# Performance work log

Measured on AMD Instinct MI355X. Metric: run time of the kernel, lower is better.

## Reference

```python
import jax, jax.numpy as jnp
import numpy as np

B = 4096      # Monte-Carlo trajectories (batch)
H = 100       # hidden_size = in_size - 1; also noise_size
T = 100       # num_timesteps
WIDTH = 256   # MLP width


def setup_inputs() -> dict:
    key = jax.random.key(0)
    ks = jax.random.split(key, 8)

    def lin(k, out_d, in_d):
        # eqx.nn.Linear default init: U(-1/sqrt(in), 1/sqrt(in)) for W and b
        lim = 1.0 / np.sqrt(in_d)
        kw, kb = jax.random.split(k)
        W = jax.random.uniform(kw, (out_d, in_d), minval=-lim, maxval=lim, dtype=jnp.float32)
        b = jax.random.uniform(kb, (out_d,), minval=-lim, maxval=lim, dtype=jnp.float32)
        return W, b

    W0, b0 = lin(ks[0], WIDTH, H + 1)
    W1, b1 = lin(ks[1], WIDTH, WIDTH)
    W2, b2 = lin(ks[2], WIDTH, WIDTH)
    W3, b3 = lin(ks[3], WIDTH, WIDTH)
    W4, b4 = lin(ks[4], 1, WIDTH)

    x0 = 1.0 + 0.1 * jax.random.normal(ks[5], (B, H), dtype=jnp.float32)
    t0 = jnp.zeros((1,), jnp.float32)
    dt = jnp.full((1,), 0.01, jnp.float32)
    return dict(x0=x0, t0=t0, dt=dt, num_timesteps=T,
                W0=W0, b0=b0, W1=W1, b1=b1, W2=W2, b2=b2, W3=W3, b3=b3, W4=W4, b4=b4)


def _mlp(params, t, x):
    # t: (1,) scalar time broadcast to batch; x: (B, H) -> (B, 1)
    W0, b0, W1, b1, W2, b2, W3, b3, W4, b4 = params
    inp = jnp.concatenate([jnp.broadcast_to(t, (x.shape[0], 1)), x], axis=-1)  # (B, H+1)
    h = jax.nn.relu(inp @ W0.T + b0)
    h = jax.nn.relu(h @ W1.T + b1)
    h = jax.nn.relu(h @ W2.T + b2)
    h = jax.nn.relu(h @ W3.T + b3)
    return h @ W4.T + b4  # (B, 1)


def _u_and_dudx(params, t, x):
    # y = u(t, x), z = du/dx via VJP with cotangent = ones (out_size == 1)
    y, vjp_fn = jax.vjp(lambda x_: _mlp(params, t, x_), x)
    (dudx,) = vjp_fn(jnp.ones_like(y))
    return y, dudx  # (B,1), (B,H)


def reference(x0, t0, dt, num_timesteps, W0, b0, W1, b1, W2, b2, W3, b3, W4, b4):
    params = (W0, b0, W1, b1, W2, b2, W3, b3, W4, b4)
    key = jax.random.key(42)
    sqdt = jnp.sqrt(dt)  # (1,)

    # initial y0, z0 evaluated at t = 0 (as in the original __call__)
    y0, z0 = _u_and_dudx(params, jnp.zeros((1,), x0.dtype), x0)

    def step(carry, _):
        i, x, y, z, k = carry
        k, k2 = jax.random.split(k)
        next_t = t0 + (i + 1.0) * dt                       # (1,)
        dW = jax.random.normal(k, x.shape, x.dtype) * sqdt  # noise_size == H
        sig = 0.4 * x                                       # sigma_fn
        x1 = x + sig * dW                                   # mu_fn == 0
        phi = 0.05 * (y - jnp.sum(x * z, axis=-1, keepdims=True))
        y1_tilde = y + phi * dt + jnp.sum(z * sig * dW, axis=-1, keepdims=True)
        y1, z1 = _u_and_dudx(params, next_t, x1)
        return (i + 1.0, x1, y1, z1, k2), (x1, y1_tilde, y1)

    carry0 = (jnp.zeros((), x0.dtype), x0, y0, z0, key)
    carry, outputs = jax.lax.scan(step, carry0, None, length=num_timesteps)
    # outputs = (xs (T,B,H), y_tildes (T,B,1), ys (T,B,1))
    return carry[1:4] + outputs  # drop step counter / key from returned carry
```

## Files before the change

kernel.cpp:

```cpp
#include <hip/hip_runtime.h>
#include <stdint.h>

#define B_TRAJ  4096
#define H_DIM   100
#define T_STEPS 100
#define ROWS    16
#define NBLK    256
#define THREADS 1024

typedef float    f32x4  __attribute__((ext_vector_type(4)));
typedef __bf16   bf16x8 __attribute__((ext_vector_type(8)));
typedef uint16_t u16x8  __attribute__((ext_vector_type(8)));
typedef uint8_t  u8x8   __attribute__((ext_vector_type(8)));

#define OB_P0F   0
#define OB_P1F   65536
#define OB_P2F   131072
#define OB_P3F   196608
#define OB_P1B   262144
#define OB_P2B   327680
#define OB_P3B   393216
#define OB_P0B   458752
#define OB_W4F8  491520
#define OB_KEYS  491776
#define PACK_TOTAL 459008
#define PACK_GRID ((PACK_TOTAL + 255) / 256)

#define WSCALE   32.0f
#define INV_WS   0.03125f
#define INV_ZS   2.44140625e-4f

__device__ __forceinline__ uint16_t f2bf(float f) {
  uint32_t u = __float_as_uint(f);
  uint32_t r = u + 0x7FFFu + ((u >> 16) & 1u);
  return (uint16_t)(r >> 16);
}
__device__ __forceinline__ float bf2f(uint16_t u) {
  return __uint_as_float(((uint32_t)u) << 16);
}
__device__ __forceinline__ uint8_t f2e4m3(float v) {
  int pk = __builtin_amdgcn_cvt_pk_fp8_f32(v, 0.0f, 0, false);
  return (uint8_t)(pk & 0xFF);
}
__device__ __forceinline__ uint32_t rotl32(uint32_t v, int d) {
  return (v << d) | (v >> (32 - d));
}

__device__ __forceinline__ void threefry2x32(uint32_t k0, uint32_t k1,
                                             uint32_t x0, uint32_t x1,
                                             uint32_t& o0, uint32_t& o1) {
  const uint32_t k2 = k0 ^ k1 ^ 0x1BD11BDAu;
  x0 += k0; x1 += k1;
  x0 += x1; x1 = rotl32(x1, 13); x1 ^= x0;
  x0 += x1; x1 = rotl32(x1, 15); x1 ^= x0;
  x0 += x1; x1 = rotl32(x1, 26); x1 ^= x0;
  x0 += x1; x1 = rotl32(x1,  6); x1 ^= x0;
  x0 += k1; x1 += k2 + 1u;
  x0 += x1; x1 = rotl32(x1, 17); x1 ^= x0;
  x0 += x1; x1 = rotl32(x1, 29); x1 ^= x0;
  x0 += x1; x1 = rotl32(x1, 16); x1 ^= x0;
  x0 += x1; x1 = rotl32(x1, 24); x1 ^= x0;
  x0 += k2; x1 += k0 + 2u;
  x0 += x1; x1 = rotl32(x1, 13); x1 ^= x0;
  x0 += x1; x1 = rotl32(x1, 15); x1 ^= x0;
  x0 += x1; x1 = rotl32(x1, 26); x1 ^= x0;
  x0 += x1; x1 = rotl32(x1,  6); x1 ^= x0;
  x0 += k0; x1 += k1 + 3u;
  x0 += x1; x1 = rotl32(x1, 17); x1 ^= x0;
  x0 += x1; x1 = rotl32(x1, 29); x1 ^= x0;
  x0 += x1; x1 = rotl32(x1, 16); x1 ^= x0;
  x0 += x1; x1 = rotl32(x1, 24); x1 ^= x0;
  x0 += k1; x1 += k2 + 4u;
  x0 += x1; x1 = rotl32(x1, 13); x1 ^= x0;
  x0 += x1; x1 = rotl32(x1, 15); x1 ^= x0;
  x0 += x1; x1 = rotl32(x1, 26); x1 ^= x0;
  x0 += x1; x1 = rotl32(x1,  6); x1 ^= x0;
  x0 += k2; x1 += k0 + 5u;
  o0 = x0; o1 = x1;
}

__device__ __forceinline__ float erfinv_f32(float x) {
  float w = -__logf(fmaf(-x, x, 1.0f));
  float p;
  if (w < 5.0f) {
    w = w - 2.5f;
    p = 2.81022636e-08f;
    p = fmaf(p, w, 3.43273939e-07f);
    p = fmaf(p, w, -3.5233877e-06f);
    p = fmaf(p, w, -4.39150654e-06f);
    p = fmaf(p, w, 0.00021858087f);
    p = fmaf(p, w, -0.00125372503f);
    p = fmaf(p, w, -0.00417768164f);
    p = fmaf(p, w, 0.246640727f);
    p = fmaf(p, w, 1.50140941f);
  } else {
    w = sqrtf(w) - 3.0f;
    p = -0.000200214257f;
    p = fmaf(p, w, 0.000100950558f);
    p = fmaf(p, w, 0.00134934322f);
    p = fmaf(p, w, -0.00367342844f);
    p = fmaf(p, w, 0.00573950773f);
    p = fmaf(p, w, -0.0076224613f);
    p = fmaf(p, w, 0.00943887047f);
    p = fmaf(p, w, 1.00167406f);
    p = fmaf(p, w, 2.83297682f);
  }
  return p * x;
}

__global__ __launch_bounds__(256) void pack_kernel(
    const float* __restrict__ W0, const float* __restrict__ W1,
    const float* __restrict__ W2, const float* __restrict__ W3,
    const float* __restrict__ W4, uint8_t* __restrict__ P) {
  const int i = blockIdx.x * 256 + threadIdx.x;
  if (i == 0) {
    uint32_t* K = (uint32_t*)(P + OB_KEYS);
    uint32_t c0 = 0u, c1 = 42u;
    for (int s = 0; s < T_STEPS; ++s) {
      uint32_t a0_, a1_, n0, n1;
      threefry2x32(c0, c1, 0u, 0u, a0_, a1_);
      threefry2x32(c0, c1, 0u, 1u, n0, n1);
      K[2 * s] = a0_; K[2 * s + 1] = a1_;
      c0 = n0; c1 = n1;
    }
  }
  if (i >= PACK_TOTAL) return;

  if (i < 32768) {
    const int e = i;
    const int kk = e & 31, n = (e >> 5) & 255, kt = e >> 13;
    const int k = kt * 32 + kk;
    const float v = (k < 101) ? W0[n * 101 + k] : 0.0f;
    ((uint16_t*)(P + OB_P0F))[e] = f2bf(v);
    return;
  }
  int j = i - 32768;
  if (j < 393216) {
    const int pk = j >> 16;
    const int e = j & 65535;
    const int kk = e & 31, n = (e >> 5) & 255, kt = e >> 13;
    const int k = kt * 32 + kk;
    float v;
    switch (pk) {
      case 0: v = W1[n * 256 + k]; break;
      case 1: v = W2[n * 256 + k]; break;
      case 2: v = W3[n * 256 + k]; break;
      case 3: v = W1[k * 256 + n]; break;
      case 4: v = W2[k * 256 + n]; break;
      default: v = W3[k * 256 + n]; break;
    }
    P[OB_P1F + j] = f2e4m3(v * WSCALE);
    return;
  }
  j -= 393216;
  if (j < 32768) {
    const int kk = j & 31, n = (j >> 5) & 127, kt = j >> 12;
    const int k = kt * 32 + kk;
    const float v = (n < 100) ? W0[k * 101 + 1 + n] : 0.0f;
    P[OB_P0B + j] = f2e4m3(v * WSCALE);
    return;
  }
  j -= 32768;
  P[OB_W4F8 + j] = f2e4m3(W4[j] * 128.0f);
}

struct SmemT {
  uint16_t actI[ROWS][136];
  uint8_t  act1[ROWS][264];
  uint8_t  act2[ROWS][264];
  uint8_t  act3[ROWS][264];
  uint8_t  act4[ROWS][264];
  uint8_t  dp4[ROWS][264];
  uint8_t  dpA[ROWS][264];
  uint8_t  dpB[ROWS][264];
  float x_s[ROWS * H_DIM];
  float z_s[ROWS * H_DIM];
  float dw_s[ROWS * H_DIM];
  float y_s[ROWS];
  uint32_t keyA[T_STEPS], keyB[T_STEPS];
};


__device__ __forceinline__ void gemm_fwd_f8(const uint8_t (*in)[264],
                                            const uint8_t* __restrict__ Pm,
                                            const float* __restrict__ bias,
                                            uint8_t (*outb)[264],
                                            int wave, int lane) {
  const int row16 = lane & 15, g = lane >> 4;
  const int c = row16 + 16 * wave;
  long bfr[8], afr[8];
#pragma unroll
  for (int kt = 0; kt < 8; ++kt)
    bfr[kt] = *reinterpret_cast<const long*>(Pm + (kt * 256 + c) * 32 + g * 8);
#pragma unroll
  for (int kt = 0; kt < 8; ++kt)
    afr[kt] = *reinterpret_cast<const long*>(&in[row16][kt * 32 + g * 8]);
  f32x4 acc = {0.f, 0.f, 0.f, 0.f};
#pragma unroll
  for (int kt = 0; kt < 8; ++kt)
    acc = __builtin_amdgcn_mfma_f32_16x16x32_fp8_fp8(afr[kt], bfr[kt], acc, 0, 0, 0);
  const float bv = bias[c];
  const float h0 = fmaxf(fmaf(acc[0], INV_WS, bv), 0.0f);
  const float h1 = fmaxf(fmaf(acc[1], INV_WS, bv), 0.0f);
  const float h2 = fmaxf(fmaf(acc[2], INV_WS, bv), 0.0f);
  const float h3 = fmaxf(fmaf(acc[3], INV_WS, bv), 0.0f);
  const int p01 = __builtin_amdgcn_cvt_pk_fp8_f32(h0, h1, 0, false);
  const int p23 = __builtin_amdgcn_cvt_pk_fp8_f32(h2, h3, 0, false);
  outb[g * 4 + 0][c] = (uint8_t)(p01 & 0xFF);
  outb[g * 4 + 1][c] = (uint8_t)((p01 >> 8) & 0xFF);
  outb[g * 4 + 2][c] = (uint8_t)(p23 & 0xFF);
  outb[g * 4 + 3][c] = (uint8_t)((p23 >> 8) & 0xFF);
}

__device__ __forceinline__ void gemm_fwd3_f8(const uint8_t (*in)[264],
                                             const uint8_t* __restrict__ Pm,
                                             const float* __restrict__ bias,
                                             const uint8_t* __restrict__ W4F8,
                                             uint8_t (*outb)[264],
                                             uint8_t (*dp4b)[264],
                                             int wave, int lane) {
  const int row16 = lane & 15, g = lane >> 4;
  const int c = row16 + 16 * wave;
  long bfr[8], afr[8];
#pragma unroll
  for (int kt = 0; kt < 8; ++kt)
    bfr[kt] = *reinterpret_cast<const long*>(Pm + (kt * 256 + c) * 32 + g * 8);
#pragma unroll
  for (int kt = 0; kt < 8; ++kt)
    afr[kt] = *reinterpret_cast<const long*>(&in[row16][kt * 32 + g * 8]);
  f32x4 acc = {0.f, 0.f, 0.f, 0.f};
#pragma unroll
  for (int kt = 0; kt < 8; ++kt)
    acc = __builtin_amdgcn_mfma_f32_16x16x32_fp8_fp8(afr[kt], bfr[kt], acc, 0, 0, 0);
  const float bv = bias[c];
  const uint8_t w4b = W4F8[c];
  const float h0 = fmaxf(fmaf(acc[0], INV_WS, bv), 0.0f);
  const float h1 = fmaxf(fmaf(acc[1], INV_WS, bv), 0.0f);
  const float h2 = fmaxf(fmaf(acc[2], INV_WS, bv), 0.0f);
  const float h3 = fmaxf(fmaf(acc[3], INV_WS, bv), 0.0f);
  const int p01 = __builtin_amdgcn_cvt_pk_fp8_f32(h0, h1, 0, false);
  const int p23 = __builtin_amdgcn_cvt_pk_fp8_f32(h2, h3, 0, false);
  outb[g * 4 + 0][c] = (uint8_t)(p01 & 0xFF);
  outb[g * 4 + 1][c] = (uint8_t)((p01 >> 8) & 0xFF);
  outb[g * 4 + 2][c] = (uint8_t)(p23 & 0xFF);
  outb[g * 4 + 3][c] = (uint8_t)((p23 >> 8) & 0xFF);
  dp4b[g * 4 + 0][c] = (h0 > 0.0f) ? w4b : (uint8_t)0;
  dp4b[g * 4 + 1][c] = (h1 > 0.0f) ? w4b : (uint8_t)0;
  dp4b[g * 4 + 2][c] = (h2 > 0.0f) ? w4b : (uint8_t)0;
  dp4b[g * 4 + 3][c] = (h3 > 0.0f) ? w4b : (uint8_t)0;
}

__device__ __forceinline__ void gemm_bwd_f8(const uint8_t (*in)[264],
                                            const uint8_t* __restrict__ Pm,
                                            const uint8_t (*mact)[264],
                                            uint8_t (*outb)[264],
                                            int wave, int lane) {
  const int row16 = lane & 15, g = lane >> 4;
  const int c = row16 + 16 * wave;
  long bfr[8], afr[8];
#pragma unroll
  for (int kt = 0; kt < 8; ++kt)
    bfr[kt] = *reinterpret_cast<const long*>(Pm + (kt * 256 + c) * 32 + g * 8);
#pragma unroll
  for (int kt = 0; kt < 8; ++kt)
    afr[kt] = *reinterpret_cast<const long*>(&in[row16][kt * 32 + g * 8]);
  f32x4 acc = {0.f, 0.f, 0.f, 0.f};
#pragma unroll
  for (int kt = 0; kt < 8; ++kt)
    acc = __builtin_amdgcn_mfma_f32_16x16x32_fp8_fp8(afr[kt], bfr[kt], acc, 0, 0, 0);
  const int p01 = __builtin_amdgcn_cvt_pk_fp8_f32(acc[0] * INV_WS, acc[1] * INV_WS, 0, false);
  const int p23 = __builtin_amdgcn_cvt_pk_fp8_f32(acc[2] * INV_WS, acc[3] * INV_WS, 0, false);
  outb[g * 4 + 0][c] = mact[g * 4 + 0][c] ? (uint8_t)(p01 & 0xFF) : (uint8_t)0;
  outb[g * 4 + 1][c] = mact[g * 4 + 1][c] ? (uint8_t)((p01 >> 8) & 0xFF) : (uint8_t)0;
  outb[g * 4 + 2][c] = mact[g * 4 + 2][c] ? (uint8_t)(p23 & 0xFF) : (uint8_t)0;
  outb[g * 4 + 3][c] = mact[g * 4 + 3][c] ? (uint8_t)((p23 >> 8) & 0xFF) : (uint8_t)0;
}

__device__ __attribute__((noinline)) void mlp_eval(
    SmemT& sm, const uint8_t* __restrict__ P,
    const float* __restrict__ b0, const float* __restrict__ b1,
    const float* __restrict__ b2, const float* __restrict__ b3,
    const float* __restrict__ W4, const float* __restrict__ b4,
    float* __restrict__ ys_out, int row0, int next_s, int blk, float sqdt) {
  const int tid = threadIdx.x;
  const int wave = tid >> 6, lane = tid & 63;
  const int row16 = lane & 15, g = lane >> 4;
  const int c = row16 + 16 * wave;

  {
    const uint16_t* P0F = (const uint16_t*)(P + OB_P0F);
    bf16x8 bfr[4], afr[4];
#pragma unroll
    for (int kt = 0; kt < 4; ++kt)
      bfr[kt] = *reinterpret_cast<const bf16x8*>(&P0F[(kt * 256 + c) * 32 + g * 8]);
#pragma unroll
    for (int kt = 0; kt < 4; ++kt)
      afr[kt] = *reinterpret_cast<const bf16x8*>(&sm.actI[row16][kt * 32 + g * 8]);
    const float bv = b0[c];
    f32x4 acc = {bv, bv, bv, bv};
#pragma unroll
    for (int kt = 0; kt < 4; ++kt)
      acc = __builtin_amdgcn_mfma_f32_16x16x32_bf16(afr[kt], bfr[kt], acc, 0, 0, 0);
    const float h0 = fmaxf(acc[0], 0.0f), h1 = fmaxf(acc[1], 0.0f);
    const float h2 = fmaxf(acc[2], 0.0f), h3 = fmaxf(acc[3], 0.0f);
    const int p01 = __builtin_amdgcn_cvt_pk_fp8_f32(h0, h1, 0, false);
    const int p23 = __builtin_amdgcn_cvt_pk_fp8_f32(h2, h3, 0, false);
    sm.act1[g * 4 + 0][c] = (uint8_t)(p01 & 0xFF);
    sm.act1[g * 4 + 1][c] = (uint8_t)((p01 >> 8) & 0xFF);
    sm.act1[g * 4 + 2][c] = (uint8_t)(p23 & 0xFF);
    sm.act1[g * 4 + 3][c] = (uint8_t)((p23 >> 8) & 0xFF);
  }
  __syncthreads();

  gemm_fwd_f8(sm.act1, P + OB_P1F, b1, sm.act2, wave, lane);
  __syncthreads();
  gemm_fwd_f8(sm.act2, P + OB_P2F, b2, sm.act3, wave, lane);
  __syncthreads();
  gemm_fwd3_f8(sm.act3, P + OB_P3F, b3, P + OB_W4F8, sm.act4, sm.dp4, wave, lane);
  __syncthreads();

  {
    const uint32_t aw = *reinterpret_cast<const uint32_t*>(&sm.act4[wave][lane * 4]);
    float sy = __builtin_amdgcn_cvt_f32_fp8(aw, 0) * W4[lane * 4 + 0]
             + __builtin_amdgcn_cvt_f32_fp8(aw, 1) * W4[lane * 4 + 1]
             + __builtin_amdgcn_cvt_f32_fp8(aw, 2) * W4[lane * 4 + 2]
             + __builtin_amdgcn_cvt_f32_fp8(aw, 3) * W4[lane * 4 + 3];
#pragma unroll
    for (int off = 32; off >= 1; off >>= 1) sy += __shfl_xor(sy, off, 64);
    if (lane == 0) {
      const float yv = sy + b4[0];
      sm.y_s[wave] = yv;
      if (ys_out) ys_out[row0 + wave] = yv;
    }
  }
  gemm_bwd_f8(sm.dp4, P + OB_P3B, sm.act3, sm.dpA, wave, lane);
  __syncthreads();

  gemm_bwd_f8(sm.dpA, P + OB_P2B, sm.act2, sm.dpB, wave, lane);
  __syncthreads();
  gemm_bwd_f8(sm.dpB, P + OB_P1B, sm.act1, sm.dpA, wave, lane);
  __syncthreads();

  if (wave < 8) {
    const uint8_t* Pm = P + OB_P0B;
    long bfr[8], afr[8];
#pragma unroll
    for (int kt = 0; kt < 8; ++kt)
      bfr[kt] = *reinterpret_cast<const long*>(Pm + (kt * 128 + c) * 32 + g * 8);
#pragma unroll
    for (int kt = 0; kt < 8; ++kt)
      afr[kt] = *reinterpret_cast<const long*>(&sm.dpA[row16][kt * 32 + g * 8]);
    f32x4 acc = {0.f, 0.f, 0.f, 0.f};
#pragma unroll
    for (int kt = 0; kt < 8; ++kt)
      acc = __builtin_amdgcn_mfma_f32_16x16x32_fp8_fp8(afr[kt], bfr[kt], acc, 0, 0, 0);
    if (c < H_DIM) {
#pragma unroll
      for (int reg = 0; reg < 4; ++reg)
        sm.z_s[(g * 4 + reg) * H_DIM + c] = acc[reg] * INV_ZS;
    }
  } else if (next_s >= 0) {
    const uint32_t ka = sm.keyA[next_s], kb = sm.keyB[next_s];
#pragma unroll
    for (int rr = 0; rr < 2; ++rr) {
      const int r = (wave - 8) * 2 + rr;
#pragma unroll
      for (int itn = 0; itn < 2; ++itn) {
        const int h = lane + itn * 64;
        if (h < H_DIM) {
          const uint32_t f = (uint32_t)(blk * (ROWS * H_DIM) + r * H_DIM + h);
          uint32_t o0, o1;
          threefry2x32(ka, kb, 0u, f, o0, o1);
          const uint32_t bits = o0 ^ o1;
          const float fr = __uint_as_float((bits >> 9) | 0x3F800000u) - 1.0f;
          const float minv = -0.99999994f;
          const float u = fmaxf(fr * 2.0f + minv, minv);
          const float n = 1.41421354f * erfinv_f32(u);
          sm.dw_s[r * H_DIM + h] = n * sqdt;
        }
      }
    }
  }
  __syncthreads();
}

__global__ __launch_bounds__(THREADS, 4) void fbsde_kernel(
    const float* __restrict__ x0, const float* __restrict__ t0p,
    const float* __restrict__ dtp,
    const float* __restrict__ b0, const float* __restrict__ b1,
    const float* __restrict__ b2, const float* __restrict__ b3,
    const float* __restrict__ W4, const float* __restrict__ b4,
    const uint8_t* __restrict__ P, float* __restrict__ out) {
  __shared__ __align__(16) SmemT sm;

  const int tid = threadIdx.x;
  const int wave = tid >> 6, lane = tid & 63;
  const int blk = blockIdx.x;
  const int row0 = blk * ROWS;

  if (tid < T_STEPS) {
    const uint32_t* K = (const uint32_t*)(P + OB_KEYS);
    sm.keyA[tid] = K[2 * tid];
    sm.keyB[tid] = K[2 * tid + 1];
  }
  for (int e = tid; e < ROWS * H_DIM; e += THREADS)
    sm.x_s[e] = x0[row0 * H_DIM + e];
  for (int e = tid; e < ROWS * 136; e += THREADS) {
    const int r = e / 136, cc = e - r * 136;
    uint16_t v = 0;
    if (cc >= 1 && cc <= H_DIM) v = f2bf(x0[(row0 + r) * H_DIM + cc - 1]);
    sm.actI[r][cc] = v;
  }
  const float t0v = t0p[0];
  const float dtv = dtp[0];
  const float sqdt = sqrtf(dtv);
  __syncthreads();

  float* const out_xfin = out;
  float* const out_yfin = out + 409600;
  float* const out_zfin = out + 413696;
  float* const out_xs   = out + 823296;
  float* const out_yt   = out + 823296 + 40960000;
  float* const out_ys   = out + 823296 + 40960000 + 409600;

  mlp_eval(sm, P, b0, b1, b2, b3, W4, b4, nullptr, row0, 0, blk, sqdt);

  for (int s = 0; s < T_STEPS; ++s) {
    const float tv = t0v + (float)(s + 1) * dtv;
    {
      const int base = wave * H_DIM;
      const int h0 = lane;
      const int h1 = lane + 64;
      const float xv0 = sm.x_s[base + h0];
      const float zv0 = sm.z_s[base + h0];
      const float dw0 = sm.dw_s[base + h0];
      float s1 = xv0 * zv0;
      float s2 = zv0 * (0.4f * xv0) * dw0;
      float xv1 = 0.f, dw1 = 0.f;
      if (h1 < H_DIM) {
        xv1 = sm.x_s[base + h1];
        const float zv1 = sm.z_s[base + h1];
        dw1 = sm.dw_s[base + h1];
        s1 += xv1 * zv1;
        s2 += zv1 * (0.4f * xv1) * dw1;
      }
#pragma unroll
      for (int off = 32; off >= 1; off >>= 1) {
        s1 += __shfl_xor(s1, off, 64);
        s2 += __shfl_xor(s2, off, 64);
      }
      if (lane == 0) {
        const float yv = sm.y_s[wave];
        const float phi = 0.05f * (yv - s1);
        out_yt[(size_t)s * B_TRAJ + row0 + wave] = yv + phi * dtv + s2;
        sm.actI[wave][0] = f2bf(tv);
      }
      {
        const float x1 = xv0 + (0.4f * xv0) * dw0;
        sm.x_s[base + h0] = x1;
        sm.actI[wave][1 + h0] = f2bf(x1);
        out_xs[(size_t)s * (B_TRAJ * H_DIM) + (size_t)(row0 + wave) * H_DIM + h0] = x1;
        if (h1 < H_DIM) {
          const float x1b = xv1 + (0.4f * xv1) * dw1;
          sm.x_s[base + h1] = x1b;
          sm.actI[wave][1 + h1] = f2bf(x1b);
          out_xs[(size_t)s * (B_TRAJ * H_DIM) + (size_t)(row0 + wave) * H_DIM + h1] = x1b;
        }
      }
    }
    __syncthreads();

    mlp_eval(sm, P, b0, b1, b2, b3, W4, b4, out_ys + (size_t)s * B_TRAJ,
             row0, (s + 1 < T_STEPS) ? s + 1 : -1, blk, sqdt);
  }

  for (int e = tid; e < ROWS * H_DIM; e += THREADS) {
    out_xfin[(size_t)row0 * H_DIM + e] = sm.x_s[e];
    out_zfin[(size_t)row0 * H_DIM + e] = sm.z_s[e];
  }
  if (tid < ROWS) out_yfin[row0 + tid] = sm.y_s[tid];
}

extern "C" void kernel_launch(void* const* d_in, const int* in_sizes, int n_in,
                              void* d_out, int out_size, void* d_ws, size_t ws_size,
                              hipStream_t stream) {
  (void)in_sizes; (void)n_in; (void)ws_size; (void)out_size;
  const float* x0 = (const float*)d_in[0];
  const float* t0 = (const float*)d_in[1];
  const float* dt = (const float*)d_in[2];
  const float* W0 = (const float*)d_in[4];
  const float* b0 = (const float*)d_in[5];
  const float* W1 = (const float*)d_in[6];
  const float* b1 = (const float*)d_in[7];
  const float* W2 = (const float*)d_in[8];
  const float* b2 = (const float*)d_in[9];
  const float* W3 = (const float*)d_in[10];
  const float* b3 = (const float*)d_in[11];
  const float* W4 = (const float*)d_in[12];
  const float* b4 = (const float*)d_in[13];
  uint8_t* P = (uint8_t*)d_ws;
  float* out = (float*)d_out;

  hipLaunchKernelGGL(pack_kernel, dim3(PACK_GRID), dim3(256), 0, stream,
                     W0, W1, W2, W3, W4, P);
  hipLaunchKernelGGL(fbsde_kernel, dim3(NBLK), dim3(THREADS), 0, stream,
                     x0, t0, dt, b0, b1, b2, b3, W4, b4, P, out);
}
```

Before: 1.212 ms.

## Halve rows per block to 8 and double blocks with 512-thread workgroups

Measured after the change: 1.878 ms. +54.9%, slower.

```diff
diff --git a/kernel.cpp b/kernel.cpp
--- a/kernel.cpp
+++ b/kernel.cpp
@@ -4,13 +4,12 @@
 #define B_TRAJ  4096
 #define H_DIM   100
 #define T_STEPS 100
-#define ROWS    16
-#define NBLK    256
-#define THREADS 1024
+#define ROWS    8
+#define NBLK    512
+#define THREADS 512
 
 typedef float    f32x4  __attribute__((ext_vector_type(4)));
 typedef __bf16   bf16x8 __attribute__((ext_vector_type(8)));
-typedef uint16_t u16x8  __attribute__((ext_vector_type(8)));
 typedef uint8_t  u8x8   __attribute__((ext_vector_type(8)));
 
 #define OB_P0F   0
@@ -34,9 +33,6 @@
   uint32_t u = __float_as_uint(f);
   uint32_t r = u + 0x7FFFu + ((u >> 16) & 1u);
   return (uint16_t)(r >> 16);
-}
-__device__ __forceinline__ float bf2f(uint16_t u) {
-  return __uint_as_float(((uint32_t)u) << 16);
 }
 __device__ __forceinline__ uint8_t f2e4m3(float v) {
   int pk = __builtin_amdgcn_cvt_pk_fp8_f32(v, 0.0f, 0, false);
@@ -165,14 +161,14 @@
 }
 
 struct SmemT {
-  uint16_t actI[ROWS][136];
-  uint8_t  act1[ROWS][264];
-  uint8_t  act2[ROWS][264];
-  uint8_t  act3[ROWS][264];
-  uint8_t  act4[ROWS][264];
-  uint8_t  dp4[ROWS][264];
-  uint8_t  dpA[ROWS][264];
-  uint8_t  dpB[ROWS][264];
+  uint16_t actI[16][136];
+  uint8_t  act1[16][264];
+  uint8_t  act2[16][264];
+  uint8_t  act3[16][264];
+  uint8_t  act4[16][264];
+  uint8_t  dp4[16][264];
+  uint8_t  dpA[16][264];
+  uint8_t  dpB[16][264];
   float x_s[ROWS * H_DIM];
   float z_s[ROWS * H_DIM];
   float dw_s[ROWS * H_DIM];
@@ -187,29 +183,39 @@
                                             uint8_t (*outb)[264],
                                             int wave, int lane) {
   const int row16 = lane & 15, g = lane >> 4;
-  const int c = row16 + 16 * wave;
-  long bfr[8], afr[8];
-#pragma unroll
-  for (int kt = 0; kt < 8; ++kt)
-    bfr[kt] = *reinterpret_cast<const long*>(Pm + (kt * 256 + c) * 32 + g * 8);
+  const int c0 = row16 + 16 * wave, c1 = c0 + 128;
+  long afr[8];
 #pragma unroll
   for (int kt = 0; kt < 8; ++kt)
     afr[kt] = *reinterpret_cast<const long*>(&in[row16][kt * 32 + g * 8]);
-  f32x4 acc = {0.f, 0.f, 0.f, 0.f};
-#pragma unroll
-  for (int kt = 0; kt < 8; ++kt)
-    acc = __builtin_amdgcn_mfma_f32_16x16x32_fp8_fp8(afr[kt], bfr[kt], acc, 0, 0, 0);
-  const float bv = bias[c];
-  const float h0 = fmaxf(fmaf(acc[0], INV_WS, bv), 0.0f);
-  const float h1 = fmaxf(fmaf(acc[1], INV_WS, bv), 0.0f);
-  const float h2 = fmaxf(fmaf(acc[2], INV_WS, bv), 0.0f);
-  const float h3 = fmaxf(fmaf(acc[3], INV_WS, bv), 0.0f);
-  const int p01 = __builtin_amdgcn_cvt_pk_fp8_f32(h0, h1, 0, false);
-  const int p23 = __builtin_amdgcn_cvt_pk_fp8_f32(h2, h3, 0, false);
-  outb[g * 4 + 0][c] = (uint8_t)(p01 & 0xFF);
-  outb[g * 4 + 1][c] = (uint8_t)((p01 >> 8) & 0xFF);
-  outb[g * 4 + 2][c] = (uint8_t)(p23 & 0xFF);
-  outb[g * 4 + 3][c] = (uint8_t)((p23 >> 8) & 0xFF);
+  f32x4 acc0 = {0.f, 0.f, 0.f, 0.f};
+#pragma unroll
+  for (int kt = 0; kt < 8; ++kt) {
+    long b = *reinterpret_cast<const long*>(Pm + (kt * 256 + c0) * 32 + g * 8);
+    acc0 = __builtin_amdgcn_mfma_f32_16x16x32_fp8_fp8(afr[kt], b, acc0, 0, 0, 0);
+  }
+  f32x4 acc1 = {0.f, 0.f, 0.f, 0.f};
+#pragma unroll
+  for (int kt = 0; kt < 8; ++kt) {
+    long b = *reinterpret_cast<const long*>(Pm + (kt * 256 + c1) * 32 + g * 8);
+    acc1 = __builtin_amdgcn_mfma_f32_16x16x32_fp8_fp8(afr[kt], b, acc1, 0, 0, 0);
+  }
+  if (g < 2) {
+    const float bv0 = bias[c0], bv1 = bias[c1];
+#pragma unroll
+    for (int reg = 0; reg < 4; reg += 2) {
+      const float a0 = fmaxf(fmaf(acc0[reg], INV_WS, bv0), 0.0f);
+      const float a1 = fmaxf(fmaf(acc0[reg + 1], INV_WS, bv0), 0.0f);
+      const float b0_ = fmaxf(fmaf(acc1[reg], INV_WS, bv1), 0.0f);
+      const float b1_ = fmaxf(fmaf(acc1[reg + 1], INV_WS, bv1), 0.0f);
+      const int pa = __builtin_amdgcn_cvt_pk_fp8_f32(a0, a1, 0, false);
+      const int pb = __builtin_amdgcn_cvt_pk_fp8_f32(b0_, b1_, 0, false);
+      outb[g * 4 + reg + 0][c0] = (uint8_t)(pa & 0xFF);
+      outb[g * 4 + reg + 1][c0] = (uint8_t)((pa >> 8) & 0xFF);
+      outb[g * 4 + reg + 0][c1] = (uint8_t)(pb & 0xFF);
+      outb[g * 4 + reg + 1][c1] = (uint8_t)((pb >> 8) & 0xFF);
+    }
+  }
 }
 
 __device__ __forceinline__ void gemm_fwd3_f8(const uint8_t (*in)[264],
@@ -220,34 +226,44 @@
                                              uint8_t (*dp4b)[264],
                                              int wave, int lane) {
   const int row16 = lane & 15, g = lane >> 4;
-  const int c = row16 + 16 * wave;
-  long bfr[8], afr[8];
-#pragma unroll
-  for (int kt = 0; kt < 8; ++kt)
-    bfr[kt] = *reinterpret_cast<const long*>(Pm + (kt * 256 + c) * 32 + g * 8);
+  const int c0 = row16 + 16 * wave, c1 = c0 + 128;
+  long afr[8];
 #pragma unroll
   for (int kt = 0; kt < 8; ++kt)
     afr[kt] = *reinterpret_cast<const long*>(&in[row16][kt * 32 + g * 8]);
-  f32x4 acc = {0.f, 0.f, 0.f, 0.f};
-#pragma unroll
-  for (int kt = 0; kt < 8; ++kt)
-    acc = __builtin_amdgcn_mfma_f32_16x16x32_fp8_fp8(afr[kt], bfr[kt], acc, 0, 0, 0);
-  const float bv = bias[c];
-  const uint8_t w4b = W4F8[c];
-  const float h0 = fmaxf(fmaf(acc[0], INV_WS, bv), 0.0f);
-  const float h1 = fmaxf(fmaf(acc[1], INV_WS, bv), 0.0f);
-  const float h2 = fmaxf(fmaf(acc[2], INV_WS, bv), 0.0f);
-  const float h3 = fmaxf(fmaf(acc[3], INV_WS, bv), 0.0f);
-  const int p01 = __builtin_amdgcn_cvt_pk_fp8_f32(h0, h1, 0, false);
-  const int p23 = __builtin_amdgcn_cvt_pk_fp8_f32(h2, h3, 0, false);
-  outb[g * 4 + 0][c] = (uint8_t)(p01 & 0xFF);
-  outb[g * 4 + 1][c] = (uint8_t)((p01 >> 8) & 0xFF);
-  outb[g * 4 + 2][c] = (uint8_t)(p23 & 0xFF);
-  outb[g * 4 + 3][c] = (uint8_t)((p23 >> 8) & 0xFF);
-  dp4b[g * 4 + 0][c] = (h0 > 0.0f) ? w4b : (uint8_t)0;
-  dp4b[g * 4 + 1][c] = (h1 > 0.0f) ? w4b : (uint8_t)0;
-  dp4b[g * 4 + 2][c] = (h2 > 0.0f) ? w4b : (uint8_t)0;
-  dp4b[g * 4 + 3][c] = (h3 > 0.0f) ? w4b : (uint8_t)0;
+  f32x4 acc0 = {0.f, 0.f, 0.f, 0.f};
+#pragma unroll
+  for (int kt = 0; kt < 8; ++kt) {
+    long b = *reinterpret_cast<const long*>(Pm + (kt * 256 + c0) * 32 + g * 8);
+    acc0 = __builtin_amdgcn_mfma_f32_16x16x32_fp8_fp8(afr[kt], b, acc0, 0, 0, 0);
+  }
+  f32x4 acc1 = {0.f, 0.f, 0.f, 0.f};
+#pragma unroll
+  for (int kt = 0; kt < 8; ++kt) {
+    long b = *reinterpret_cast<const long*>(Pm + (kt * 256 + c1) * 32 + g * 8);
+    acc1 = __builtin_amdgcn_mfma_f32_16x16x32_fp8_fp8(afr[kt], b, acc1, 0, 0, 0);
+  }
+  if (g < 2) {
+    const float bv0 = bias[c0], bv1 = bias[c1];
+    const uint8_t w40 = W4F8[c0], w41 = W4F8[c1];
+#pragma unroll
+    for (int reg = 0; reg < 4; reg += 2) {
+      const float a0 = fmaxf(fmaf(acc0[reg], INV_WS, bv0), 0.0f);
+      const float a1 = fmaxf(fmaf(acc0[reg + 1], INV_WS, bv0), 0.0f);
+      const float b0_ = fmaxf(fmaf(acc1[reg], INV_WS, bv1), 0.0f);
+      const float b1_ = fmaxf(fmaf(acc1[reg + 1], INV_WS, bv1), 0.0f);
+      const int pa = __builtin_amdgcn_cvt_pk_fp8_f32(a0, a1, 0, false);
+      const int pb = __builtin_amdgcn_cvt_pk_fp8_f32(b0_, b1_, 0, false);
+      outb[g * 4 + reg + 0][c0] = (uint8_t)(pa & 0xFF);
+      outb[g * 4 + reg + 1][c0] = (uint8_t)((pa >> 8) & 0xFF);
+      outb[g * 4 + reg + 0][c1] = (uint8_t)(pb & 0xFF);
+      outb[g * 4 + reg + 1][c1] = (uint8_t)((pb >> 8) & 0xFF);
+      dp4b[g * 4 + reg + 0][c0] = (a0 > 0.0f) ? w40 : (uint8_t)0;
+      dp4b[g * 4 + reg + 1][c0] = (a1 > 0.0f) ? w40 : (uint8_t)0;
+      dp4b[g * 4 + reg + 0][c1] = (b0_ > 0.0f) ? w41 : (uint8_t)0;
+      dp4b[g * 4 + reg + 1][c1] = (b1_ > 0.0f) ? w41 : (uint8_t)0;
+    }
+  }
 }
 
 __device__ __forceinline__ void gemm_bwd_f8(const uint8_t (*in)[264],
@@ -256,24 +272,37 @@
                                             uint8_t (*outb)[264],
                                             int wave, int lane) {
   const int row16 = lane & 15, g = lane >> 4;
-  const int c = row16 + 16 * wave;
-  long bfr[8], afr[8];
-#pragma unroll
-  for (int kt = 0; kt < 8; ++kt)
-    bfr[kt] = *reinterpret_cast<const long*>(Pm + (kt * 256 + c) * 32 + g * 8);
+  const int c0 = row16 + 16 * wave, c1 = c0 + 128;
+  long afr[8];
 #pragma unroll
   for (int kt = 0; kt < 8; ++kt)
     afr[kt] = *reinterpret_cast<const long*>(&in[row16][kt * 32 + g * 8]);
-  f32x4 acc = {0.f, 0.f, 0.f, 0.f};
-#pragma unroll
-  for (int kt = 0; kt < 8; ++kt)
-    acc = __builtin_amdgcn_mfma_f32_16x16x32_fp8_fp8(afr[kt], bfr[kt], acc, 0, 0, 0);
-  const int p01 = __builtin_amdgcn_cvt_pk_fp8_f32(acc[0] * INV_WS, acc[1] * INV_WS, 0, false);
-  const int p23 = __builtin_amdgcn_cvt_pk_fp8_f32(acc[2] * INV_WS, acc[3] * INV_WS, 0, false);
-  outb[g * 4 + 0][c] = mact[g * 4 + 0][c] ? (uint8_t)(p01 & 0xFF) : (uint8_t)0;
-  outb[g * 4 + 1][c] = mact[g * 4 + 1][c] ? (uint8_t)((p01 >> 8) & 0xFF) : (uint8_t)0;
-  outb[g * 4 + 2][c] = mact[g * 4 + 2][c] ? (uint8_t)(p23 & 0xFF) : (uint8_t)0;
-  outb[g * 4 + 3][c] = mact[g * 4 + 3][c] ? (uint8_t)((p23 >> 8) & 0xFF) : (uint8_t)0;
+  f32x4 acc0 = {0.f, 0.f, 0.f, 0.f};
+#pragma unroll
+  for (int kt = 0; kt < 8; ++kt) {
+    long b = *reinterpret_cast<const long*>(Pm + (kt * 256 + c0) * 32 + g * 8);
+    acc0 = __builtin_amdgcn_mfma_f32_16x16x32_fp8_fp8(afr[kt], b, acc0, 0, 0, 0);
+  }
+  f32x4 acc1 = {0.f, 0.f, 0.f, 0.f};
+#pragma unroll
+  for (int kt = 0; kt < 8; ++kt) {
+    long b = *reinterpret_cast<const long*>(Pm + (kt * 256 + c1) * 32 + g * 8);
+    acc1 = __builtin_amdgcn_mfma_f32_16x16x32_fp8_fp8(afr[kt], b, acc1, 0, 0, 0);
+  }
+  if (g < 2) {
+#pragma unroll
+    for (int reg = 0; reg < 4; reg += 2) {
+      const int r0 = g * 4 + reg, r1 = r0 + 1;
+      const int pa = __builtin_amdgcn_cvt_pk_fp8_f32(acc0[reg] * INV_WS,
+                                                     acc0[reg + 1] * INV_WS, 0, false);
+      const int pb = __builtin_amdgcn_cvt_pk_fp8_f32(acc1[reg] * INV_WS,
+                                                     acc1[reg + 1] * INV_WS, 0, false);
+      outb[r0][c0] = mact[r0][c0] ? (uint8_t)(pa & 0xFF) : (uint8_t)0;
+      outb[r1][c0] = mact[r1][c0] ? (uint8_t)((pa >> 8) & 0xFF) : (uint8_t)0;
+      outb[r0][c1] = mact[r0][c1] ? (uint8_t)(pb & 0xFF) : (uint8_t)0;
+      outb[r1][c1] = mact[r1][c1] ? (uint8_t)((pb >> 8) & 0xFF) : (uint8_t)0;
+    }
+  }
 }
 
 __device__ __attribute__((noinline)) void mlp_eval(
@@ -285,30 +314,43 @@
   const int tid = threadIdx.x;
   const int wave = tid >> 6, lane = tid & 63;
   const int row16 = lane & 15, g = lane >> 4;
-  const int c = row16 + 16 * wave;
+  const int c0 = row16 + 16 * wave;
 
   {
     const uint16_t* P0F = (const uint16_t*)(P + OB_P0F);
-    bf16x8 bfr[4], afr[4];
-#pragma unroll
-    for (int kt = 0; kt < 4; ++kt)
-      bfr[kt] = *reinterpret_cast<const bf16x8*>(&P0F[(kt * 256 + c) * 32 + g * 8]);
+    const int c1 = c0 + 128;
+    bf16x8 afr[4];
 #pragma unroll
     for (int kt = 0; kt < 4; ++kt)
       afr[kt] = *reinterpret_cast<const bf16x8*>(&sm.actI[row16][kt * 32 + g * 8]);
-    const float bv = b0[c];
-    f32x4 acc = {bv, bv, bv, bv};
-#pragma unroll
-    for (int kt = 0; kt < 4; ++kt)
-      acc = __builtin_amdgcn_mfma_f32_16x16x32_bf16(afr[kt], bfr[kt], acc, 0, 0, 0);
-    const float h0 = fmaxf(acc[0], 0.0f), h1 = fmaxf(acc[1], 0.0f);
-    const float h2 = fmaxf(acc[2], 0.0f), h3 = fmaxf(acc[3], 0.0f);
-    const int p01 = __builtin_amdgcn_cvt_pk_fp8_f32(h0, h1, 0, false);
-    const int p23 = __builtin_amdgcn_cvt_pk_fp8_f32(h2, h3, 0, false);
-    sm.act1[g * 4 + 0][c] = (uint8_t)(p01 & 0xFF);
-    sm.act1[g * 4 + 1][c] = (uint8_t)((p01 >> 8) & 0xFF);
-    sm.act1[g * 4 + 2][c] = (uint8_t)(p23 & 0xFF);
-    sm.act1[g * 4 + 3][c] = (uint8_t)((p23 >> 8) & 0xFF);
+    f32x4 acc0 = {0.f, 0.f, 0.f, 0.f};
+#pragma unroll
+    for (int kt = 0; kt < 4; ++kt) {
+      bf16x8 b = *reinterpret_cast<const bf16x8*>(&P0F[(kt * 256 + c0) * 32 + g * 8]);
+      acc0 = __builtin_amdgcn_mfma_f32_16x16x32_bf16(afr[kt], b, acc0, 0, 0, 0);
+    }
+    f32x4 acc1 = {0.f, 0.f, 0.f, 0.f};
+#pragma unroll
+    for (int kt = 0; kt < 4; ++kt) {
+      bf16x8 b = *reinterpret_cast<const bf16x8*>(&P0F[(kt * 256 + c1) * 32 + g * 8]);
+      acc1 = __builtin_amdgcn_mfma_f32_16x16x32_bf16(afr[kt], b, acc1, 0, 0, 0);
+    }
+    if (g < 2) {
+      const float bv0 = b0[c0], bv1 = b0[c1];
+#pragma unroll
+      for (int reg = 0; reg < 4; reg += 2) {
+        const float a0 = fmaxf(acc0[reg] + bv0, 0.0f);
+        const float a1 = fmaxf(acc0[reg + 1] + bv0, 0.0f);
+        const float v0 = fmaxf(acc1[reg] + bv1, 0.0f);
+        const float v1 = fmaxf(acc1[reg + 1] + bv1, 0.0f);
+        const int pa = __builtin_amdgcn_cvt_pk_fp8_f32(a0, a1, 0, false);
+        const int pb = __builtin_amdgcn_cvt_pk_fp8_f32(v0, v1, 0, false);
+        sm.act1[g * 4 + reg + 0][c0] = (uint8_t)(pa & 0xFF);
+        sm.act1[g * 4 + reg + 1][c0] = (uint8_t)((pa >> 8) & 0xFF);
+        sm.act1[g * 4 + reg + 0][c1] = (uint8_t)(pb & 0xFF);
+        sm.act1[g * 4 + reg + 1][c1] = (uint8_t)((pb >> 8) & 0xFF);
+      }
+    }
   }
   __syncthreads();
 
@@ -341,44 +383,38 @@
   gemm_bwd_f8(sm.dpB, P + OB_P1B, sm.act1, sm.dpA, wave, lane);
   __syncthreads();
 
-  if (wave < 8) {
+  {
     const uint8_t* Pm = P + OB_P0B;
-    long bfr[8], afr[8];
-#pragma unroll
-    for (int kt = 0; kt < 8; ++kt)
-      bfr[kt] = *reinterpret_cast<const long*>(Pm + (kt * 128 + c) * 32 + g * 8);
+    long afr[8];
 #pragma unroll
     for (int kt = 0; kt < 8; ++kt)
       afr[kt] = *reinterpret_cast<const long*>(&sm.dpA[row16][kt * 32 + g * 8]);
     f32x4 acc = {0.f, 0.f, 0.f, 0.f};
 #pragma unroll
-    for (int kt = 0; kt < 8; ++kt)
-      acc = __builtin_amdgcn_mfma_f32_16x16x32_fp8_fp8(afr[kt], bfr[kt], acc, 0, 0, 0);
-    if (c < H_DIM) {
+    for (int kt = 0; kt < 8; ++kt) {
+      long b = *reinterpret_cast<const long*>(Pm + (kt * 128 + c0) * 32 + g * 8);
+      acc = __builtin_amdgcn_mfma_f32_16x16x32_fp8_fp8(afr[kt], b, acc, 0, 0, 0);
+    }
+
+    if (next_s >= 0) {
+      const uint32_t ka = sm.keyA[next_s], kb = sm.keyB[next_s];
+      for (int e = tid; e < ROWS * H_DIM; e += THREADS) {
+        const uint32_t f = (uint32_t)(blk * (ROWS * H_DIM) + e);
+        uint32_t o0, o1;
+        threefry2x32(ka, kb, 0u, f, o0, o1);
+        const uint32_t bits = o0 ^ o1;
+        const float fr = __uint_as_float((bits >> 9) | 0x3F800000u) - 1.0f;
+        const float minv = -0.99999994f;
+        const float u = fmaxf(fr * 2.0f + minv, minv);
+        const float n = 1.41421354f * erfinv_f32(u);
+        sm.dw_s[e] = n * sqdt;
+      }
+    }
+
+    if (g < 2 && c0 < H_DIM) {
 #pragma unroll
       for (int reg = 0; reg < 4; ++reg)
-        sm.z_s[(g * 4 + reg) * H_DIM + c] = acc[reg] * INV_ZS;
-    }
-  } else if (next_s >= 0) {
-    const uint32_t ka = sm.keyA[next_s], kb = sm.keyB[next_s];
-#pragma unroll
-    for (int rr = 0; rr < 2; ++rr) {
-      const int r = (wave - 8) * 2 + rr;
-#pragma unroll
-      for (int itn = 0; itn < 2; ++itn) {
-        const int h = lane + itn * 64;
-        if (h < H_DIM) {
-          const uint32_t f = (uint32_t)(blk * (ROWS * H_DIM) + r * H_DIM + h);
-          uint32_t o0, o1;
-          threefry2x32(ka, kb, 0u, f, o0, o1);
-          const uint32_t bits = o0 ^ o1;
-          const float fr = __uint_as_float((bits >> 9) | 0x3F800000u) - 1.0f;
-          const float minv = -0.99999994f;
-          const float u = fmaxf(fr * 2.0f + minv, minv);
-          const float n = 1.41421354f * erfinv_f32(u);
-          sm.dw_s[r * H_DIM + h] = n * sqdt;
-        }
-      }
+        sm.z_s[(g * 4 + reg) * H_DIM + c0] = acc[reg] * INV_ZS;
     }
   }
   __syncthreads();
@@ -405,11 +441,16 @@
   }
   for (int e = tid; e < ROWS * H_DIM; e += THREADS)
     sm.x_s[e] = x0[row0 * H_DIM + e];
-  for (int e = tid; e < ROWS * 136; e += THREADS) {
+  for (int e = tid; e < 16 * 136; e += THREADS) {
     const int r = e / 136, cc = e - r * 136;
     uint16_t v = 0;
-    if (cc >= 1 && cc <= H_DIM) v = f2bf(x0[(row0 + r) * H_DIM + cc - 1]);
+    if (r < ROWS && cc >= 1 && cc <= H_DIM)
+      v = f2bf(x0[(row0 + r) * H_DIM + cc - 1]);
     sm.actI[r][cc] = v;
+  }
+  {
+    uint32_t* pz = (uint32_t*)&sm.act1[0][0];
+    for (int e = tid; e < 7 * 16 * 264 / 4; e += THREADS) pz[e] = 0u;
   }
   const float t0v = t0p[0];
   const float dtv = dtp[0];
```

## Halve rows per block to double grid size, padding MFMA tiles to 16 rows

Applied to the files above, without the earlier changes.

Measured after the change: 2.224 ms. +83.5%, slower.

```diff
diff --git a/kernel.cpp b/kernel.cpp
--- a/kernel.cpp
+++ b/kernel.cpp
@@ -4,13 +4,12 @@
 #define B_TRAJ  4096
 #define H_DIM   100
 #define T_STEPS 100
-#define ROWS    16
-#define NBLK    256
+#define ROWS    8
+#define NBLK    512
 #define THREADS 1024
 
 typedef float    f32x4  __attribute__((ext_vector_type(4)));
 typedef __bf16   bf16x8 __attribute__((ext_vector_type(8)));
-typedef uint16_t u16x8  __attribute__((ext_vector_type(8)));
 typedef uint8_t  u8x8   __attribute__((ext_vector_type(8)));
 
 #define OB_P0F   0
@@ -34,9 +33,6 @@
   uint32_t u = __float_as_uint(f);
   uint32_t r = u + 0x7FFFu + ((u >> 16) & 1u);
   return (uint16_t)(r >> 16);
-}
-__device__ __forceinline__ float bf2f(uint16_t u) {
-  return __uint_as_float(((uint32_t)u) << 16);
 }
 __device__ __forceinline__ uint8_t f2e4m3(float v) {
   int pk = __builtin_amdgcn_cvt_pk_fp8_f32(v, 0.0f, 0, false);
@@ -165,14 +161,14 @@
 }
 
 struct SmemT {
-  uint16_t actI[ROWS][136];
-  uint8_t  act1[ROWS][264];
-  uint8_t  act2[ROWS][264];
-  uint8_t  act3[ROWS][264];
-  uint8_t  act4[ROWS][264];
-  uint8_t  dp4[ROWS][264];
-  uint8_t  dpA[ROWS][264];
-  uint8_t  dpB[ROWS][264];
+  uint16_t actI[16][136];
+  uint8_t  act1[16][264];
+  uint8_t  act2[16][264];
+  uint8_t  act3[16][264];
+  uint8_t  act4[16][264];
+  uint8_t  dp4[16][264];
+  uint8_t  dpA[16][264];
+  uint8_t  dpB[16][264];
   float x_s[ROWS * H_DIM];
   float z_s[ROWS * H_DIM];
   float dw_s[ROWS * H_DIM];
@@ -199,17 +195,19 @@
 #pragma unroll
   for (int kt = 0; kt < 8; ++kt)
     acc = __builtin_amdgcn_mfma_f32_16x16x32_fp8_fp8(afr[kt], bfr[kt], acc, 0, 0, 0);
-  const float bv = bias[c];
-  const float h0 = fmaxf(fmaf(acc[0], INV_WS, bv), 0.0f);
-  const float h1 = fmaxf(fmaf(acc[1], INV_WS, bv), 0.0f);
-  const float h2 = fmaxf(fmaf(acc[2], INV_WS, bv), 0.0f);
-  const float h3 = fmaxf(fmaf(acc[3], INV_WS, bv), 0.0f);
-  const int p01 = __builtin_amdgcn_cvt_pk_fp8_f32(h0, h1, 0, false);
-  const int p23 = __builtin_amdgcn_cvt_pk_fp8_f32(h2, h3, 0, false);
-  outb[g * 4 + 0][c] = (uint8_t)(p01 & 0xFF);
-  outb[g * 4 + 1][c] = (uint8_t)((p01 >> 8) & 0xFF);
-  outb[g * 4 + 2][c] = (uint8_t)(p23 & 0xFF);
-  outb[g * 4 + 3][c] = (uint8_t)((p23 >> 8) & 0xFF);
+  if (g < 2) {
+    const float bv = bias[c];
+    const float h0 = fmaxf(fmaf(acc[0], INV_WS, bv), 0.0f);
+    const float h1 = fmaxf(fmaf(acc[1], INV_WS, bv), 0.0f);
+    const float h2 = fmaxf(fmaf(acc[2], INV_WS, bv), 0.0f);
+    const float h3 = fmaxf(fmaf(acc[3], INV_WS, bv), 0.0f);
+    const int p01 = __builtin_amdgcn_cvt_pk_fp8_f32(h0, h1, 0, false);
+    const int p23 = __builtin_amdgcn_cvt_pk_fp8_f32(h2, h3, 0, false);
+    outb[g * 4 + 0][c] = (uint8_t)(p01 & 0xFF);
+    outb[g * 4 + 1][c] = (uint8_t)((p01 >> 8) & 0xFF);
+    outb[g * 4 + 2][c] = (uint8_t)(p23 & 0xFF);
+    outb[g * 4 + 3][c] = (uint8_t)((p23 >> 8) & 0xFF);
+  }
 }
 
 __device__ __forceinline__ void gemm_fwd3_f8(const uint8_t (*in)[264],
@@ -232,22 +230,24 @@
 #pragma unroll
   for (int kt = 0; kt < 8; ++kt)
     acc = __builtin_amdgcn_mfma_f32_16x16x32_fp8_fp8(afr[kt], bfr[kt], acc, 0, 0, 0);
-  const float bv = bias[c];
-  const uint8_t w4b = W4F8[c];
-  const float h0 = fmaxf(fmaf(acc[0], INV_WS, bv), 0.0f);
-  const float h1 = fmaxf(fmaf(acc[1], INV_WS, bv), 0.0f);
-  const float h2 = fmaxf(fmaf(acc[2], INV_WS, bv), 0.0f);
-  const float h3 = fmaxf(fmaf(acc[3], INV_WS, bv), 0.0f);
-  const int p01 = __builtin_amdgcn_cvt_pk_fp8_f32(h0, h1, 0, false);
-  const int p23 = __builtin_amdgcn_cvt_pk_fp8_f32(h2, h3, 0, false);
-  outb[g * 4 + 0][c] = (uint8_t)(p01 & 0xFF);
-  outb[g * 4 + 1][c] = (uint8_t)((p01 >> 8) & 0xFF);
-  outb[g * 4 + 2][c] = (uint8_t)(p23 & 0xFF);
-  outb[g * 4 + 3][c] = (uint8_t)((p23 >> 8) & 0xFF);
-  dp4b[g * 4 + 0][c] = (h0 > 0.0f) ? w4b : (uint8_t)0;
-  dp4b[g * 4 + 1][c] = (h1 > 0.0f) ? w4b : (uint8_t)0;
-  dp4b[g * 4 + 2][c] = (h2 > 0.0f) ? w4b : (uint8_t)0;
-  dp4b[g * 4 + 3][c] = (h3 > 0.0f) ? w4b : (uint8_t)0;
+  if (g < 2) {
+    const float bv = bias[c];
+    const uint8_t w4b = W4F8[c];
+    const float h0 = fmaxf(fmaf(acc[0], INV_WS, bv), 0.0f);
+    const float h1 = fmaxf(fmaf(acc[1], INV_WS, bv), 0.0f);
+    const float h2 = fmaxf(fmaf(acc[2], INV_WS, bv), 0.0f);
+    const float h3 = fmaxf(fmaf(acc[3], INV_WS, bv), 0.0f);
+    const int p01 = __builtin_amdgcn_cvt_pk_fp8_f32(h0, h1, 0, false);
+    const int p23 = __builtin_amdgcn_cvt_pk_fp8_f32(h2, h3, 0, false);
+    outb[g * 4 + 0][c] = (uint8_t)(p01 & 0xFF);
+    outb[g * 4 + 1][c] = (uint8_t)((p01 >> 8) & 0xFF);
+    outb[g * 4 + 2][c] = (uint8_t)(p23 & 0xFF);
+    outb[g * 4 + 3][c] = (uint8_t)((p23 >> 8) & 0xFF);
+    dp4b[g * 4 + 0][c] = (h0 > 0.0f) ? w4b : (uint8_t)0;
+    dp4b[g * 4 + 1][c] = (h1 > 0.0f) ? w4b : (uint8_t)0;
+    dp4b[g * 4 + 2][c] = (h2 > 0.0f) ? w4b : (uint8_t)0;
+    dp4b[g * 4 + 3][c] = (h3 > 0.0f) ? w4b : (uint8_t)0;
+  }
 }
 
 __device__ __forceinline__ void gemm_bwd_f8(const uint8_t (*in)[264],
@@ -268,12 +268,14 @@
 #pragma unroll
   for (int kt = 0; kt < 8; ++kt)
     acc = __builtin_amdgcn_mfma_f32_16x16x32_fp8_fp8(afr[kt], bfr[kt], acc, 0, 0, 0);
-  const int p01 = __builtin_amdgcn_cvt_pk_fp8_f32(acc[0] * INV_WS, acc[1] * INV_WS, 0, false);
-  const int p23 = __builtin_amdgcn_cvt_pk_fp8_f32(acc[2] * INV_WS, acc[3] * INV_WS, 0, false);
-  outb[g * 4 + 0][c] = mact[g * 4 + 0][c] ? (uint8_t)(p01 & 0xFF) : (uint8_t)0;
-  outb[g * 4 + 1][c] = mact[g * 4 + 1][c] ? (uint8_t)((p01 >> 8) & 0xFF) : (uint8_t)0;
-  outb[g * 4 + 2][c] = mact[g * 4 + 2][c] ? (uint8_t)(p23 & 0xFF) : (uint8_t)0;
-  outb[g * 4 + 3][c] = mact[g * 4 + 3][c] ? (uint8_t)((p23 >> 8) & 0xFF) : (uint8_t)0;
+  if (g < 2) {
+    const int p01 = __builtin_amdgcn_cvt_pk_fp8_f32(acc[0] * INV_WS, acc[1] * INV_WS, 0, false);
+    const int p23 = __builtin_amdgcn_cvt_pk_fp8_f32(acc[2] * INV_WS, acc[3] * INV_WS, 0, false);
+    outb[g * 4 + 0][c] = mact[g * 4 + 0][c] ? (uint8_t)(p01 & 0xFF) : (uint8_t)0;
+    outb[g * 4 + 1][c] = mact[g * 4 + 1][c] ? (uint8_t)((p01 >> 8) & 0xFF) : (uint8_t)0;
+    outb[g * 4 + 2][c] = mact[g * 4 + 2][c] ? (uint8_t)(p23 & 0xFF) : (uint8_t)0;
+    outb[g * 4 + 3][c] = mact[g * 4 + 3][c] ? (uint8_t)((p23 >> 8) & 0xFF) : (uint8_t)0;
+  }
 }
 
 __device__ __attribute__((noinline)) void mlp_eval(
@@ -296,19 +298,21 @@
 #pragma unroll
     for (int kt = 0; kt < 4; ++kt)
       afr[kt] = *reinterpret_cast<const bf16x8*>(&sm.actI[row16][kt * 32 + g * 8]);
-    const float bv = b0[c];
-    f32x4 acc = {bv, bv, bv, bv};
+    f32x4 acc = {0.f, 0.f, 0.f, 0.f};
 #pragma unroll
     for (int kt = 0; kt < 4; ++kt)
       acc = __builtin_amdgcn_mfma_f32_16x16x32_bf16(afr[kt], bfr[kt], acc, 0, 0, 0);
-    const float h0 = fmaxf(acc[0], 0.0f), h1 = fmaxf(acc[1], 0.0f);
-    const float h2 = fmaxf(acc[2], 0.0f), h3 = fmaxf(acc[3], 0.0f);
-    const int p01 = __builtin_amdgcn_cvt_pk_fp8_f32(h0, h1, 0, false);
-    const int p23 = __builtin_amdgcn_cvt_pk_fp8_f32(h2, h3, 0, false);
-    sm.act1[g * 4 + 0][c] = (uint8_t)(p01 & 0xFF);
-    sm.act1[g * 4 + 1][c] = (uint8_t)((p01 >> 8) & 0xFF);
-    sm.act1[g * 4 + 2][c] = (uint8_t)(p23 & 0xFF);
-    sm.act1[g * 4 + 3][c] = (uint8_t)((p23 >> 8) & 0xFF);
+    if (g < 2) {
+      const float bv = b0[c];
+      const float h0 = fmaxf(acc[0] + bv, 0.0f), h1 = fmaxf(acc[1] + bv, 0.0f);
+      const float h2 = fmaxf(acc[2] + bv, 0.0f), h3 = fmaxf(acc[3] + bv, 0.0f);
+      const int p01 = __builtin_amdgcn_cvt_pk_fp8_f32(h0, h1, 0, false);
+      const int p23 = __builtin_amdgcn_cvt_pk_fp8_f32(h2, h3, 0, false);
+      sm.act1[g * 4 + 0][c] = (uint8_t)(p01 & 0xFF);
+      sm.act1[g * 4 + 1][c] = (uint8_t)((p01 >> 8) & 0xFF);
+      sm.act1[g * 4 + 2][c] = (uint8_t)(p23 & 0xFF);
+      sm.act1[g * 4 + 3][c] = (uint8_t)((p23 >> 8) & 0xFF);
+    }
   }
   __syncthreads();
 
@@ -319,7 +323,7 @@
   gemm_fwd3_f8(sm.act3, P + OB_P3F, b3, P + OB_W4F8, sm.act4, sm.dp4, wave, lane);
   __syncthreads();
 
-  {
+  if (wave < ROWS) {
     const uint32_t aw = *reinterpret_cast<const uint32_t*>(&sm.act4[wave][lane * 4]);
     float sy = __builtin_amdgcn_cvt_f32_fp8(aw, 0) * W4[lane * 4 + 0]
              + __builtin_amdgcn_cvt_f32_fp8(aw, 1) * W4[lane * 4 + 1]
@@ -354,31 +358,23 @@
 #pragma unroll
     for (int kt = 0; kt < 8; ++kt)
       acc = __builtin_amdgcn_mfma_f32_16x16x32_fp8_fp8(afr[kt], bfr[kt], acc, 0, 0, 0);
-    if (c < H_DIM) {
+    if (g < 2 && c < H_DIM) {
 #pragma unroll
       for (int reg = 0; reg < 4; ++reg)
         sm.z_s[(g * 4 + reg) * H_DIM + c] = acc[reg] * INV_ZS;
     }
   } else if (next_s >= 0) {
     const uint32_t ka = sm.keyA[next_s], kb = sm.keyB[next_s];
-#pragma unroll
-    for (int rr = 0; rr < 2; ++rr) {
-      const int r = (wave - 8) * 2 + rr;
-#pragma unroll
-      for (int itn = 0; itn < 2; ++itn) {
-        const int h = lane + itn * 64;
-        if (h < H_DIM) {
-          const uint32_t f = (uint32_t)(blk * (ROWS * H_DIM) + r * H_DIM + h);
-          uint32_t o0, o1;
-          threefry2x32(ka, kb, 0u, f, o0, o1);
-          const uint32_t bits = o0 ^ o1;
-          const float fr = __uint_as_float((bits >> 9) | 0x3F800000u) - 1.0f;
-          const float minv = -0.99999994f;
-          const float u = fmaxf(fr * 2.0f + minv, minv);
-          const float n = 1.41421354f * erfinv_f32(u);
-          sm.dw_s[r * H_DIM + h] = n * sqdt;
-        }
-      }
+    for (int e = tid - 512; e < ROWS * H_DIM; e += 512) {
+      const uint32_t f = (uint32_t)(blk * (ROWS * H_DIM) + e);
+      uint32_t o0, o1;
+      threefry2x32(ka, kb, 0u, f, o0, o1);
+      const uint32_t bits = o0 ^ o1;
+      const float fr = __uint_as_float((bits >> 9) | 0x3F800000u) - 1.0f;
+      const float minv = -0.99999994f;
+      const float u = fmaxf(fr * 2.0f + minv, minv);
+      const float n = 1.41421354f * erfinv_f32(u);
+      sm.dw_s[e] = n * sqdt;
     }
   }
   __syncthreads();
@@ -405,11 +401,16 @@
   }
   for (int e = tid; e < ROWS * H_DIM; e += THREADS)
     sm.x_s[e] = x0[row0 * H_DIM + e];
-  for (int e = tid; e < ROWS * 136; e += THREADS) {
+  for (int e = tid; e < 16 * 136; e += THREADS) {
     const int r = e / 136, cc = e - r * 136;
     uint16_t v = 0;
-    if (cc >= 1 && cc <= H_DIM) v = f2bf(x0[(row0 + r) * H_DIM + cc - 1]);
+    if (r < ROWS && cc >= 1 && cc <= H_DIM)
+      v = f2bf(x0[(row0 + r) * H_DIM + cc - 1]);
     sm.actI[r][cc] = v;
+  }
+  {
+    uint32_t* pz = (uint32_t*)&sm.act1[0][0];
+    for (int e = tid; e < 7 * 16 * 264 / 4; e += THREADS) pz[e] = 0u;
   }
   const float t0v = t0p[0];
   const float dtv = dtp[0];
@@ -427,7 +428,7 @@
 
   for (int s = 0; s < T_STEPS; ++s) {
     const float tv = t0v + (float)(s + 1) * dtv;
-    {
+    if (wave < ROWS) {
       const int base = wave * H_DIM;
       const int h0 = lane;
       const int h1 = lane + 64;
```
